# Kernel optimization log

Measured on AMD Instinct MI355X. Metric: run time of the kernel, lower is better.

The kernel has to match this reference:

```python
import jax, jax.numpy as jnp
import numpy as np

B, C, N = 2, 1024, 80
D = 3 * C + 2  # 3074 token dim
DFF = 2048     # torch TransformerEncoderLayer default dim_feedforward
HW = 224
REFINE = 3
EPS = 1e-5


def _layernorm(x, g, b):
    m = jnp.mean(x, axis=-1, keepdims=True)
    v = jnp.mean((x - m) ** 2, axis=-1, keepdims=True)
    return g * (x - m) / jnp.sqrt(v + EPS) + b


def _pos_encoding(seq_len, dim):
    pos = jnp.arange(seq_len, dtype=jnp.float32)[:, None]
    div = jnp.exp(jnp.arange(0, dim, 2, dtype=jnp.float32) * (-np.log(10000.0) / dim))
    pe = jnp.zeros((seq_len, dim), dtype=jnp.float32)
    pe = pe.at[:, 0::2].set(jnp.sin(pos * div)).at[:, 1::2].set(jnp.cos(pos * div))
    return pe


def _forward(pre_f, curr_f, first_f, ln_g, ln_b, ipw, ipb, opw, opb,
             n1g, n1b, l1w, l1b, l2w, l2b, n2g, n2b, ow, ob,
             prev_b, first_b):
    # --- vectorized find_best_shift: batched circular L1 correlation ---
    idx = (jnp.arange(N)[None, :] - jnp.arange(N)[:, None]) % N  # [shift, pos]
    rolled = first_b[:, idx]                                     # [B, N, N, 2]
    dist = jnp.abs(prev_b[:, None] - rolled).sum(axis=(-1, -2))  # [B, N]
    best = jnp.argmin(dist, axis=1)                              # first min, like torch loop
    roll_idx = (jnp.arange(N)[None, :] - best[:, None]) % N      # [B, N]
    first_b = jax.vmap(lambda fb, ri: fb[ri])(first_b, roll_idx)

    # --- bilinear upsample to 224x224 (F.interpolate, align_corners=False) ---
    up = lambda f: jax.image.resize(f, (f.shape[0], f.shape[1], HW, HW), method='bilinear')
    pre_up, curr_up, first_up = up(pre_f), up(curr_f), up(first_f)

    # --- vectorized get_bou_features: [B,N,C] gather ---
    gather = jax.vmap(lambda f, b: f[:, b[:, 0], b[:, 1]].T)
    pre_q = gather(pre_up, prev_b)      # [B, N, C]
    first_q = gather(first_up, first_b)  # [B, N, C]

    pe = _pos_encoding(N, D)
    curr = prev_b.astype(jnp.float32)
    scale = 1.0 / jnp.sqrt(jnp.float32(D))
    results = []
    for _ in range(REFINE):
        bf = gather(curr_up, curr.astype(jnp.int32))          # [B, N, C]
        tokens = jnp.concatenate([pre_q, bf, curr, first_q], axis=-1)  # [B, N, D]
        tokens = _layernorm(tokens, ln_g, ln_b)
        tokens = tokens + pe[None]
        # --- TransformerEncoderLayer (post-norm, nhead=1, relu, eval/no dropout) ---
        qkv = tokens @ ipw.T + ipb
        q, k, v = jnp.split(qkv, 3, axis=-1)
        attn = jax.nn.softmax(jnp.einsum('bqd,bkd->bqk', q, k) * scale, axis=-1)
        a = jnp.einsum('bqk,bkd->bqd', attn, v) @ opw.T + opb
        x = _layernorm(tokens + a, n1g, n1b)
        ff = jax.nn.relu(x @ l1w.T + l1b) @ l2w.T + l2b
        x = _layernorm(x + ff, n2g, n2b)
        out = x @ ow.T + ob                                   # [B, N, 1026]
        curr = jnp.clip(curr + out[..., C:], 0.0, 223.0)
        pre_q = pre_q + out[..., :C]
        results.append(curr)
    return jnp.stack(results)  # [REFINE, B, N, 2]


def setup_inputs() -> dict:
    key = jax.random.key(0)
    ks = jax.random.split(key, 12)
    f = lambda i, s: jax.random.normal(ks[i], s, dtype=jnp.float32)
    w = lambda i, s: 0.02 * jax.random.normal(ks[i], s, dtype=jnp.float32)
    return {
        'pre_img_features': f(0, (B, C, 14, 14)),
        'curr_img_features': f(1, (B, C, 14, 14)),
        'first_img_features': f(2, (B, C, 14, 14)),
        'previous_boundary': jax.random.randint(ks[3], (B, N, 2), 0, HW),
        'first_boundary': jax.random.randint(ks[4], (B, N, 2), 0, HW),
        'ln_g': jnp.ones((D,), jnp.float32), 'ln_b': jnp.zeros((D,), jnp.float32),
        'in_proj_w': w(5, (3 * D, D)), 'in_proj_b': jnp.zeros((3 * D,), jnp.float32),
        'out_proj_w': w(6, (D, D)), 'out_proj_b': jnp.zeros((D,), jnp.float32),
        'norm1_g': jnp.ones((D,), jnp.float32), 'norm1_b': jnp.zeros((D,), jnp.float32),
        'lin1_w': w(7, (DFF, D)), 'lin1_b': jnp.zeros((DFF,), jnp.float32),
        'lin2_w': w(8, (D, DFF)), 'lin2_b': jnp.zeros((D,), jnp.float32),
        'norm2_g': jnp.ones((D,), jnp.float32), 'norm2_b': jnp.zeros((D,), jnp.float32),
        'out_w': w(9, (C + 2, D)), 'out_b': jnp.zeros((C + 2,), jnp.float32),
    }


def reference(pre_img_features, curr_img_features, first_img_features,
              previous_boundary, first_boundary,
              ln_g, ln_b, in_proj_w, in_proj_b, out_proj_w, out_proj_b,
              norm1_g, norm1_b, lin1_w, lin1_b, lin2_w, lin2_b,
              norm2_g, norm2_b, out_w, out_b):
    return _forward(pre_img_features, curr_img_features, first_img_features,
                    ln_g, ln_b, in_proj_w, in_proj_b, out_proj_w, out_proj_b,
                    norm1_g, norm1_b, lin1_w, lin1_b, lin2_w, lin2_b,
                    norm2_g, norm2_b, out_w, out_b,
                    previous_boundary, first_boundary)
```

## Files before the change

kernel.cpp:

```cpp
#include <hip/hip_runtime.h>
#include <math.h>

#define B_    2
#define C_    1024
#define N_    80
#define D_    3074
#define DFF_  2048
#define OD_   1026
#define QKV_  9222
#define M_    160
#define EPS_  1e-5f
#define KPD_  3104

#define SQKV 4
#define PQKV 25
#define SOP  8
#define POP  13
#define SFF1 11
#define PFF1 9
#define SFF2 8
#define PFF2 8
#define SHD  11
#define PHD  9

typedef __attribute__((ext_vector_type(8))) short bf16x8;
typedef __attribute__((ext_vector_type(4))) float f32x4;

__device__ inline short f2bf(float f) {
    unsigned u = __float_as_uint(f);
    u += 0x7fffu + ((u >> 16) & 1u);
    return (short)(u >> 16);
}

__device__ inline int pack2bf(float lo, float hi) {
    return (int)(unsigned short)f2bf(lo) | ((int)(unsigned short)f2bf(hi) << 16);
}

__device__ inline float wave_sum(float v) {
#pragma unroll
    for (int off = 32; off > 0; off >>= 1) v += __shfl_down(v, off, 64);
    return v;
}

__device__ inline void block_reduce_2(float& s, float& s2, float* red) {
    int tid = threadIdx.x;
    int lane = tid & 63, wid = tid >> 6;
    s = wave_sum(s);
    s2 = wave_sum(s2);
    if (lane == 0) { red[wid] = s; red[4 + wid] = s2; }
    __syncthreads();
    if (tid == 0) {
        red[8] = red[0] + red[1] + red[2] + red[3];
        red[9] = red[4] + red[5] + red[6] + red[7];
    }
    __syncthreads();
    s = red[8]; s2 = red[9];
}

__device__ inline void bilin_setup(int p, int& i0, int& i1, float& t) {
    float s = (p + 0.5f) * 0.0625f - 0.5f;
    s = fminf(fmaxf(s, 0.0f), 13.0f);
    i0 = (int)s;
    t = s - (float)i0;
    i1 = min(i0 + 1, 13);
}

__device__ inline float bilin_tap(const float* f, int y0, int y1, float ty,
                                  int x0, int x1, float tx) {
    float a = f[y0 * 14 + x0], b = f[y0 * 14 + x1];
    float c = f[y1 * 14 + x0], d = f[y1 * 14 + x1];
    return (1.f - ty) * ((1.f - tx) * a + tx * b) + ty * ((1.f - tx) * c + tx * d);
}

__global__ __launch_bounds__(128) void align_kernel(const int* __restrict__ prev_b,
                                                    const int* __restrict__ first_b,
                                                    int* __restrict__ fb_al) {
    int b = blockIdx.x;
    int tid = threadIdx.x;
    __shared__ int dist[N_];
    __shared__ int bestIdx;
    if (tid < N_) {
        int s = 0;
        for (int j = 0; j < N_; ++j) {
            int src = (j - tid) % N_;
            if (src < 0) src += N_;
            int dy = prev_b[(b * N_ + j) * 2] - first_b[(b * N_ + src) * 2];
            int dx = prev_b[(b * N_ + j) * 2 + 1] - first_b[(b * N_ + src) * 2 + 1];
            s += abs(dy) + abs(dx);
        }
        dist[tid] = s;
    }
    __syncthreads();
    if (tid == 0) {
        int best = 0, bd = dist[0];
        for (int i = 1; i < N_; ++i)
            if (dist[i] < bd) { bd = dist[i]; best = i; }
        bestIdx = best;
    }
    __syncthreads();
    if (tid < N_) {
        int src = (tid - bestIdx) % N_;
        if (src < 0) src += N_;
        fb_al[(b * N_ + tid) * 2]     = first_b[(b * N_ + src) * 2];
        fb_al[(b * N_ + tid) * 2 + 1] = first_b[(b * N_ + src) * 2 + 1];
    }
}

__global__ __launch_bounds__(256) void gather_init_kernel(
        const float* __restrict__ pre_f, const float* __restrict__ first_f,
        const int* __restrict__ prev_b, const int* __restrict__ fb_al,
        float* __restrict__ pre_q, float* __restrict__ first_q,
        float* __restrict__ curr) {
    int m = blockIdx.x;
    int b = m / N_;
    int tid = threadIdx.x;
    int py = prev_b[m * 2], px = prev_b[m * 2 + 1];
    int fy = fb_al[m * 2], fx = fb_al[m * 2 + 1];
    int py0, py1, px0, px1, fy0, fy1, fx0, fx1;
    float pty, ptx, fty, ftx;
    bilin_setup(py, py0, py1, pty);
    bilin_setup(px, px0, px1, ptx);
    bilin_setup(fy, fy0, fy1, fty);
    bilin_setup(fx, fx0, fx1, ftx);
    for (int c = tid; c < C_; c += 256) {
        const float* fp = pre_f + (size_t)(b * C_ + c) * 196;
        const float* ff = first_f + (size_t)(b * C_ + c) * 196;
        pre_q[(size_t)m * C_ + c]   = bilin_tap(fp, py0, py1, pty, px0, px1, ptx);
        first_q[(size_t)m * C_ + c] = bilin_tap(ff, fy0, fy1, fty, fx0, fx1, ftx);
    }
    if (tid < 2) curr[m * 2 + tid] = (float)prev_b[m * 2 + tid];
}

__global__ __launch_bounds__(256) void pe_kernel(float* __restrict__ pe) {
    int n = blockIdx.x;
    const float negLogDivD = -logf(10000.0f) / (float)D_;
    for (int d = threadIdx.x; d < D_; d += 256) {
        int kk = d >> 1;
        float ang = (float)n * expf((float)(2 * kk) * negLogDivD);
        pe[(size_t)n * D_ + d] = (d & 1) ? cosf(ang) : sinf(ang);
    }
}

__global__ __launch_bounds__(256) void tokens_kernel(
        const float* __restrict__ curr_f, const float* __restrict__ pre_q,
        const float* __restrict__ first_q, const float* __restrict__ curr,
        const float* __restrict__ ln_g, const float* __restrict__ ln_b,
        const float* __restrict__ pe_tab,
        float* __restrict__ tokens, short* __restrict__ tokens_bf) {
    int m = blockIdx.x;
    int b = m / N_;
    int n = m % N_;
    int tid = threadIdx.x;
    __shared__ float bf[C_];
    __shared__ float red[10];

    float cy = curr[m * 2], cx = curr[m * 2 + 1];
    int iy = (int)cy, ix = (int)cx;
    int y0, y1, x0, x1;
    float ty, tx;
    bilin_setup(iy, y0, y1, ty);
    bilin_setup(ix, x0, x1, tx);
    for (int c = tid; c < C_; c += 256) {
        const float* f = curr_f + (size_t)(b * C_ + c) * 196;
        bf[c] = bilin_tap(f, y0, y1, ty, x0, x1, tx);
    }
    __syncthreads();

    float s = 0.f, s2 = 0.f;
    for (int d = tid; d < D_; d += 256) {
        float v;
        if (d < C_)            v = pre_q[(size_t)m * C_ + d];
        else if (d < 2 * C_)   v = bf[d - C_];
        else if (d == 2 * C_)  v = cy;
        else if (d == 2*C_+1)  v = cx;
        else                   v = first_q[(size_t)m * C_ + (d - 2 * C_ - 2)];
        s += v; s2 += v * v;
    }
    block_reduce_2(s, s2, red);
    float mean = s / (float)D_;
    float var = s2 / (float)D_ - mean * mean;
    float inv = rsqrtf(var + EPS_);

    for (int d = tid; d < KPD_; d += 256) {
        if (d < D_) {
            float v;
            if (d < C_)            v = pre_q[(size_t)m * C_ + d];
            else if (d < 2 * C_)   v = bf[d - C_];
            else if (d == 2 * C_)  v = cy;
            else if (d == 2*C_+1)  v = cx;
            else                   v = first_q[(size_t)m * C_ + (d - 2 * C_ - 2)];
            float ln = ln_g[d] * (v - mean) * inv + ln_b[d];
            float val = ln + pe_tab[(size_t)n * D_ + d];
            tokens[(size_t)m * D_ + d] = val;
            tokens_bf[(size_t)m * KPD_ + d] = f2bf(val);
        } else {
            tokens_bf[(size_t)m * KPD_ + d] = 0;
        }
    }
}

__global__ __launch_bounds__(256) void wpack2(const float* __restrict__ w,
                                              short* __restrict__ o,
                                              int K, int O, int nch, int ntiles) {
    int gw = (int)((blockIdx.x * 256 + threadIdx.x) >> 6);
    if (gw >= ntiles) return;
    int lane = threadIdx.x & 63;
    int strip = gw / nch, chunk = gw - strip * nch;
    int row = strip * 16 + (lane >> 2);
    int k0 = chunk * 32 + (lane & 3) * 8;
    float f[8];
    if (row < O && k0 + 8 <= K) {
        const float* src = w + (size_t)row * K + k0;
        float2 a = *(const float2*)(src);
        float2 b = *(const float2*)(src + 2);
        float2 c = *(const float2*)(src + 4);
        float2 d = *(const float2*)(src + 6);
        f[0]=a.x; f[1]=a.y; f[2]=b.x; f[3]=b.y;
        f[4]=c.x; f[5]=c.y; f[6]=d.x; f[7]=d.y;
    } else {
#pragma unroll
        for (int j = 0; j < 8; ++j) {
            int k = k0 + j;
            f[j] = (row < O && k < K) ? w[(size_t)row * K + k] : 0.f;
        }
    }
    int p0 = pack2bf(f[0], f[1]);
    int p1 = pack2bf(f[2], f[3]);
    int p2 = pack2bf(f[4], f[5]);
    int p3 = pack2bf(f[6], f[7]);
    int src = (lane & 15) * 4 + (lane >> 4);
    int4 out;
    out.x = __shfl(p0, src, 64);
    out.y = __shfl(p1, src, 64);
    out.z = __shfl(p2, src, 64);
    out.w = __shfl(p3, src, 64);
    *(int4*)(o + (size_t)gw * 512 + (size_t)lane * 8) = out;
}

template <int SW>
__global__ __launch_bounds__(512) void gemm_stage(
        const short* __restrict__ A, const short* __restrict__ Wp,
        const float* __restrict__ bias, float* __restrict__ part,
        int KpA, int nch, int O, int per) {
    int cs = blockIdx.y * per;
    int ce = min(nch, cs + per);
    if (cs >= ce) return;
    int tid = threadIdx.x;
    int lane = tid & 63, wave = tid >> 6;
    int col = lane & 15, quad = lane >> 4;
    int s0 = (blockIdx.x * 8 + wave) * SW;

    __shared__ short lbuf[2][160 * 32];

    int m0 = tid >> 2, p8 = (tid & 3) * 8;
    int m1 = (tid + 512) >> 2;
    const short* a0 = A + (size_t)m0 * KpA + p8;
    const short* a1 = A + (size_t)m1 * KpA + p8;
    bf16x8 sr0, sr1;

    f32x4 acc[SW][10];
#pragma unroll
    for (int j = 0; j < SW; ++j)
#pragma unroll
        for (int t = 0; t < 10; ++t)
#pragma unroll
            for (int r = 0; r < 4; ++r) acc[j][t][r] = 0.f;

    const short* wbase[SW];
#pragma unroll
    for (int j = 0; j < SW; ++j)
        wbase[j] = Wp + (size_t)(s0 + j) * nch * 512 + (size_t)lane * 8;
    bf16x8 wc[SW], wn[SW];

    sr0 = *(const bf16x8*)(a0 + (size_t)cs * 32);
    if (tid < 128) sr1 = *(const bf16x8*)(a1 + (size_t)cs * 32);
#pragma unroll
    for (int j = 0; j < SW; ++j)
        wc[j] = *(const bf16x8*)(wbase[j] + (size_t)cs * 512);
    *(bf16x8*)(&lbuf[0][m0 * 32 + p8]) = sr0;
    if (tid < 128) *(bf16x8*)(&lbuf[0][m1 * 32 + p8]) = sr1;
    __syncthreads();

    int cur = 0;
    for (int c = cs; c < ce; ++c) {
        bool more = (c + 1) < ce;
        if (more) {
            sr0 = *(const bf16x8*)(a0 + (size_t)(c + 1) * 32);
            if (tid < 128) sr1 = *(const bf16x8*)(a1 + (size_t)(c + 1) * 32);
#pragma unroll
            for (int j = 0; j < SW; ++j)
                wn[j] = *(const bf16x8*)(wbase[j] + (size_t)(c + 1) * 512);
        }
#pragma unroll
        for (int t = 0; t < 10; ++t) {
            bf16x8 af = *(const bf16x8*)(&lbuf[cur][t * 512 + col * 32 + quad * 8]);
#pragma unroll
            for (int j = 0; j < SW; ++j)
                acc[j][t] = __builtin_amdgcn_mfma_f32_16x16x32_bf16(af, wc[j], acc[j][t], 0, 0, 0);
        }
        if (more) {
            *(bf16x8*)(&lbuf[cur ^ 1][m0 * 32 + p8]) = sr0;
            if (tid < 128) *(bf16x8*)(&lbuf[cur ^ 1][m1 * 32 + p8]) = sr1;
        }
        __syncthreads();
#pragma unroll
        for (int j = 0; j < SW; ++j) wc[j] = wn[j];
        cur ^= 1;
    }

    float* pout = part + (size_t)blockIdx.y * M_ * O;
#pragma unroll
    for (int j = 0; j < SW; ++j) {
        int oc = (s0 + j) * 16 + col;
        if (oc < O) {
            float bv = (blockIdx.y == 0) ? bias[oc] : 0.f;
#pragma unroll
            for (int t = 0; t < 10; ++t)
#pragma unroll
                for (int r = 0; r < 4; ++r)
                    pout[(size_t)(t * 16 + quad * 4 + r) * O + oc] = acc[j][t][r] + bv;
        }
    }
}

__global__ __launch_bounds__(256) void gemm_mfma_sk(
        const short* __restrict__ A, const float* __restrict__ Wf,
        const float* __restrict__ bias, float* __restrict__ Cout,
        int K, int KpA, int O, int KC) {
    int kc0 = blockIdx.y * KC;
    if (kc0 >= K) return;
    int kend = min(K, kc0 + KC);

    int lane = threadIdx.x & 63;
    int wave = threadIdx.x >> 6;
    int col  = lane & 15;
    int quad = lane >> 4;
    int o0 = blockIdx.x * 128 + wave * 32 + col;
    int o1 = o0 + 16;
    int oc0 = min(o0, O - 1), oc1 = min(o1, O - 1);

    const float* wrow0 = Wf + (size_t)oc0 * K + quad * 8;
    const float* wrow1 = Wf + (size_t)oc1 * K + quad * 8;
    const short* abase = A + (size_t)col * KpA + quad * 8;

    f32x4 acc0[10], acc1[10];
#pragma unroll
    for (int t = 0; t < 10; ++t)
#pragma unroll
        for (int r = 0; r < 4; ++r) { acc0[t][r] = 0.f; acc1[t][r] = 0.f; }

    int nfull = (kend - kc0) >> 5;
    bf16x8 aCur[10];
    float2 wCur[8];
    if (nfull > 0) {
#pragma unroll
        for (int t = 0; t < 10; ++t)
            aCur[t] = *(const bf16x8*)(abase + (size_t)t * 16 * KpA + kc0);
#pragma unroll
        for (int j = 0; j < 4; ++j) {
            wCur[j]     = *(const float2*)(wrow0 + kc0 + 2 * j);
            wCur[4 + j] = *(const float2*)(wrow1 + kc0 + 2 * j);
        }
    }
    for (int i = 0; i < nfull; ++i) {
        bf16x8 aNxt[10];
        float2 wNxt[8];
        if (i + 1 < nfull) {
            int kn = kc0 + (i + 1) * 32;
#pragma unroll
            for (int t = 0; t < 10; ++t)
                aNxt[t] = *(const bf16x8*)(abase + (size_t)t * 16 * KpA + kn);
#pragma unroll
            for (int j = 0; j < 4; ++j) {
                wNxt[j]     = *(const float2*)(wrow0 + kn + 2 * j);
                wNxt[4 + j] = *(const float2*)(wrow1 + kn + 2 * j);
            }
        }
        bf16x8 b0, b1;
#pragma unroll
        for (int j = 0; j < 4; ++j) {
            b0[2*j] = f2bf(wCur[j].x);     b0[2*j+1] = f2bf(wCur[j].y);
            b1[2*j] = f2bf(wCur[4+j].x);   b1[2*j+1] = f2bf(wCur[4+j].y);
        }
#pragma unroll
        for (int t = 0; t < 10; ++t) {
            acc0[t] = __builtin_amdgcn_mfma_f32_16x16x32_bf16(aCur[t], b0, acc0[t], 0, 0, 0);
            acc1[t] = __builtin_amdgcn_mfma_f32_16x16x32_bf16(aCur[t], b1, acc1[t], 0, 0, 0);
        }
#pragma unroll
        for (int t = 0; t < 10; ++t) aCur[t] = aNxt[t];
#pragma unroll
        for (int j = 0; j < 8; ++j) wCur[j] = wNxt[j];
    }
    int kmain = kc0 + nfull * 32;
    if (kmain < kend) {
        bf16x8 b0, b1;
#pragma unroll
        for (int j = 0; j < 8; ++j) {
            int k = kmain + quad * 8 + j;
            b0[j] = (k < kend) ? f2bf(Wf[(size_t)oc0 * K + k]) : (short)0;
            b1[j] = (k < kend) ? f2bf(Wf[(size_t)oc1 * K + k]) : (short)0;
        }
#pragma unroll
        for (int t = 0; t < 10; ++t) {
            bf16x8 af = *(const bf16x8*)(abase + (size_t)t * 16 * KpA + kmain);
            acc0[t] = __builtin_amdgcn_mfma_f32_16x16x32_bf16(af, b0, acc0[t], 0, 0, 0);
            acc1[t] = __builtin_amdgcn_mfma_f32_16x16x32_bf16(af, b1, acc1[t], 0, 0, 0);
        }
    }
    if (o0 < O) {
        float bv = (blockIdx.y == 0) ? bias[o0] : 0.f;
#pragma unroll
        for (int t = 0; t < 10; ++t)
#pragma unroll
            for (int r = 0; r < 4; ++r)
                atomicAdd(&Cout[(size_t)(t * 16 + quad * 4 + r) * O + o0], acc0[t][r] + bv);
    }
    if (o1 < O) {
        float bv = (blockIdx.y == 0) ? bias[o1] : 0.f;
#pragma unroll
        for (int t = 0; t < 10; ++t)
#pragma unroll
            for (int r = 0; r < 4; ++r)
                atomicAdd(&Cout[(size_t)(t * 16 + quad * 4 + r) * O + o1], acc1[t][r] + bv);
    }
}

__global__ __launch_bounds__(256) void relu_cvt_kernel(const float* __restrict__ in,
                                                       int S, size_t sstr,
                                                       short* __restrict__ out,
                                                       int n) {
    int i = blockIdx.x * 256 + threadIdx.x;
    if (i < n) {
        float v = 0.f;
        for (int s = 0; s < S; ++s) v += in[(size_t)s * sstr + i];
        out[i] = f2bf(fmaxf(v, 0.f));
    }
}

__global__ __launch_bounds__(256) void qkv_cvt_kernel(const float* __restrict__ part,
                                                      int S,
                                                      short* __restrict__ q_bf,
                                                      short* __restrict__ k_bf,
                                                      short* __restrict__ v_bf) {
    int mb = blockIdx.x;
    int b = mb / 96, q = mb % 96;
    if (q >= N_) {
        for (int d = threadIdx.x; d < KPD_; d += 256)
            v_bf[((size_t)b * 96 + q) * KPD_ + d] = 0;
        return;
    }
    int m = b * N_ + q;
    for (int d = threadIdx.x; d < KPD_; d += 256) {
        short qv = 0, kv = 0, vv = 0;
        if (d < D_) {
            float qf = 0.f, kf = 0.f, vf = 0.f;
            for (int s = 0; s < S; ++s) {
                const float* p = part + (size_t)s * M_ * QKV_ + (size_t)m * QKV_;
                qf += p[d]; kf += p[D_ + d]; vf += p[2 * D_ + d];
            }
            qv = f2bf(qf); kv = f2bf(kf); vv = f2bf(vf);
        }
        q_bf[(size_t)m * KPD_ + d] = qv;
        k_bf[(size_t)m * KPD_ + d] = kv;
        v_bf[((size_t)b * 96 + q) * KPD_ + d] = vv;
    }
}

__global__ __launch_bounds__(256) void attn_sc(const short* __restrict__ q_bf,
                                               const short* __restrict__ k_bf,
                                               short* __restrict__ p_bf) {
    int bi = blockIdx.x;
    int b = bi / 5, qt = bi % 5;
    int lane = threadIdx.x & 63, wave = threadIdx.x >> 6;
    int col = lane & 15, quad = lane >> 4;
    const short* qbase = q_bf + (size_t)(b * N_ + qt * 16 + col) * KPD_ + quad * 8;
    const short* kb = k_bf + (size_t)(b * N_ + col) * KPD_ + quad * 8;

    f32x4 acc[5];
#pragma unroll
    for (int kt = 0; kt < 5; ++kt)
#pragma unroll
        for (int r = 0; r < 4; ++r) acc[kt][r] = 0.f;

    int c0 = wave * 25, c1 = min(97, c0 + 25);
    for (int c = c0; c < c1; ++c) {
        bf16x8 af = *(const bf16x8*)(qbase + (size_t)c * 32);
#pragma unroll
        for (int kt = 0; kt < 5; ++kt) {
            bf16x8 kf = *(const bf16x8*)(kb + (size_t)(kt * 16) * KPD_ + (size_t)c * 32);
            acc[kt] = __builtin_amdgcn_mfma_f32_16x16x32_bf16(af, kf, acc[kt], 0, 0, 0);
        }
    }

    __shared__ f32x4 red[4][5][64];
    __shared__ float sl[16][80];
#pragma unroll
    for (int kt = 0; kt < 5; ++kt) red[wave][kt][lane] = acc[kt];
    __syncthreads();
    float scale = rsqrtf((float)D_);
    for (int item = threadIdx.x; item < 320; item += 256) {
        int kt = item >> 6, l2 = item & 63;
        int c2 = l2 & 15, q2 = l2 >> 4;
        f32x4 v = red[0][kt][l2];
#pragma unroll
        for (int w = 1; w < 4; ++w)
#pragma unroll
            for (int r = 0; r < 4; ++r) v[r] += red[w][kt][l2][r];
#pragma unroll
        for (int r = 0; r < 4; ++r)
            sl[q2 * 4 + r][kt * 16 + c2] = v[r] * scale;
    }
    __syncthreads();

    int r = wave * 4 + (lane >> 4);
    int cb = lane & 15;
    float v[5];
    float mx = -1e30f;
#pragma unroll
    for (int i = 0; i < 5; ++i) { v[i] = sl[r][cb + 16 * i]; mx = fmaxf(mx, v[i]); }
#pragma unroll
    for (int off = 1; off < 16; off <<= 1) mx = fmaxf(mx, __shfl_xor(mx, off, 64));
    float e[5];
    float sum = 0.f;
#pragma unroll
    for (int i = 0; i < 5; ++i) { e[i] = expf(v[i] - mx); sum += e[i]; }
#pragma unroll
    for (int off = 1; off < 16; off <<= 1) sum += __shfl_xor(sum, off, 64);
    float rs = 1.0f / sum;
    size_t m96 = (size_t)(b * N_ + qt * 16 + r) * 96;
#pragma unroll
    for (int i = 0; i < 5; ++i) p_bf[m96 + cb + 16 * i] = f2bf(e[i] * rs);
    p_bf[m96 + 80 + cb] = 0;
}

__global__ __launch_bounds__(256) void av_mfma(const short* __restrict__ p_bf,
                                               const short* __restrict__ v_bf,
                                               short* __restrict__ av_bf) {
    int bi = blockIdx.x;
    int b = bi / 49, g = bi % 49;
    int lane = threadIdx.x & 63, wave = threadIdx.x >> 6;
    int dtile = g * 4 + wave;
    if (dtile >= 194) return;
    int d0 = dtile * 16;
    int col = lane & 15, quad = lane >> 4;
    const short* pbase = p_bf + (size_t)b * N_ * 96 + quad * 8;
    const short* vb = v_bf + (size_t)b * 96 * KPD_ + d0 + col;
    f32x4 acc[5];
#pragma unroll
    for (int t = 0; t < 5; ++t)
#pragma unroll
        for (int r = 0; r < 4; ++r) acc[t][r] = 0.f;
#pragma unroll
    for (int c = 0; c < 3; ++c) {
        bf16x8 bf8;
#pragma unroll
        for (int j = 0; j < 8; ++j)
            bf8[j] = vb[(size_t)(c * 32 + quad * 8 + j) * KPD_];
#pragma unroll
        for (int t = 0; t < 5; ++t) {
            bf16x8 af = *(const bf16x8*)(pbase + (size_t)(t * 16 + col) * 96 + c * 32);
            acc[t] = __builtin_amdgcn_mfma_f32_16x16x32_bf16(af, bf8, acc[t], 0, 0, 0);
        }
    }
#pragma unroll
    for (int t = 0; t < 5; ++t)
#pragma unroll
        for (int r = 0; r < 4; ++r)
            av_bf[(size_t)(b * N_ + t * 16 + quad * 4 + r) * KPD_ + d0 + col] = f2bf(acc[t][r]);
}

template <bool WF32>
__global__ __launch_bounds__(256) void ln_kernel(const float* __restrict__ xin,
                                                 int S, size_t sstr,
                                                 const float* __restrict__ res,
                                                 const float* __restrict__ g,
                                                 const float* __restrict__ bta,
                                                 float* __restrict__ outf,
                                                 short* __restrict__ outb) {
    int m = blockIdx.x;
    int tid = threadIdx.x;
    __shared__ float red[10];
    const float* xr = xin + (size_t)m * D_;
    const float* rr = res + (size_t)m * D_;
    float vv[13];
    float s = 0.f, s2 = 0.f;
#pragma unroll
    for (int i = 0; i < 13; ++i) {
        int d = tid + i * 256;
        float v = 0.f;
        if (d < D_) {
            v = rr[d];
            for (int sp = 0; sp < S; ++sp) v += xr[(size_t)sp * sstr + d];
            s += v; s2 += v * v;
        }
        vv[i] = v;
    }
    block_reduce_2(s, s2, red);
    float mean = s / (float)D_;
    float var = s2 / (float)D_ - mean * mean;
    float inv = rsqrtf(var + EPS_);
#pragma unroll
    for (int i = 0; i < 13; ++i) {
        int d = tid + i * 256;
        if (d < D_) {
            float y = g[d] * (vv[i] - mean) * inv + bta[d];
            if (WF32) outf[(size_t)m * D_ + d] = y;
            outb[(size_t)m * KPD_ + d] = f2bf(y);
        } else if (d < KPD_) {
            outb[(size_t)m * KPD_ + d] = 0;
        }
    }
}

__global__ __launch_bounds__(256) void update_kernel(const float* __restrict__ part,
                                                     int S, size_t sstr,
                                                     float* __restrict__ curr,
                                                     float* __restrict__ pre_q,
                                                     float* __restrict__ results) {
    int m = blockIdx.x;
    int tid = threadIdx.x;
    const float* pr = part + (size_t)m * OD_;
    for (int c = tid; c < C_; c += 256) {
        float v = 0.f;
        for (int s = 0; s < S; ++s) v += pr[(size_t)s * sstr + c];
        pre_q[(size_t)m * C_ + c] += v;
    }
    if (tid < 2) {
        float v = 0.f;
        for (int s = 0; s < S; ++s) v += pr[(size_t)s * sstr + C_ + tid];
        float nc = curr[m * 2 + tid] + v;
        nc = fminf(fmaxf(nc, 0.f), 223.f);
        curr[m * 2 + tid] = nc;
        results[m * 2 + tid] = nc;
    }
}

extern "C" void kernel_launch(void* const* d_in, const int* in_sizes, int n_in,
                              void* d_out, int out_size, void* d_ws, size_t ws_size,
                              hipStream_t stream) {
    const float* pre_f   = (const float*)d_in[0];
    const float* curr_f  = (const float*)d_in[1];
    const float* first_f = (const float*)d_in[2];
    const int*   prev_b  = (const int*)d_in[3];
    const int*   first_b = (const int*)d_in[4];
    const float* ln_g    = (const float*)d_in[5];
    const float* ln_b    = (const float*)d_in[6];
    const float* ipw     = (const float*)d_in[7];
    const float* ipb     = (const float*)d_in[8];
    const float* opw     = (const float*)d_in[9];
    const float* opb     = (const float*)d_in[10];
    const float* n1g     = (const float*)d_in[11];
    const float* n1b     = (const float*)d_in[12];
    const float* l1w     = (const float*)d_in[13];
    const float* l1b     = (const float*)d_in[14];
    const float* l2w     = (const float*)d_in[15];
    const float* l2b     = (const float*)d_in[16];
    const float* n2g     = (const float*)d_in[17];
    const float* n2b     = (const float*)d_in[18];
    const float* ow      = (const float*)d_in[19];
    const float* ob      = (const float*)d_in[20];
    float* outp = (float*)d_out;

    float* wf = (float*)d_ws;
    size_t off = 0;
    int*   fb_al   = (int*)(wf + off); off += 320;
    float* curr    = wf + off;         off += 320;
    float* pre_q   = wf + off;         off += (size_t)M_ * C_;
    float* first_q = wf + off;         off += (size_t)M_ * C_;
    float* tokens  = wf + off;         off += (size_t)M_ * D_;
    float* xbuf    = wf + off;         off += (size_t)M_ * D_;
    float* pe_tab  = wf + off;         off += (size_t)N_ * D_;
    short* tokens_bf = (short*)(wf + off); off += (size_t)M_ * KPD_ / 2;
    short* x_bf      = (short*)(wf + off); off += (size_t)M_ * KPD_ / 2;
    short* x2_bf     = (short*)(wf + off); off += (size_t)M_ * KPD_ / 2;
    short* av_bf     = (short*)(wf + off); off += (size_t)M_ * KPD_ / 2;
    short* ff1_bf    = (short*)(wf + off); off += (size_t)M_ * DFF_ / 2;
    short* q_bf      = (short*)(wf + off); off += (size_t)M_ * KPD_ / 2;
    short* k_bf      = (short*)(wf + off); off += (size_t)M_ * KPD_ / 2;
    short* v_bf      = (short*)(wf + off); off += (size_t)B_ * 96 * KPD_ / 2;
    short* p_bf      = (short*)(wf + off); off += (size_t)M_ * 96 / 2;
    size_t commonF = off;

    size_t o2 = commonF;
    short* ipw_p2 = (short*)(wf + o2); o2 += (size_t)592 * 97 * 256;
    short* opw_p2 = (short*)(wf + o2); o2 += (size_t)208 * 97 * 256;
    short* l1w_p2 = (short*)(wf + o2); o2 += (size_t)128 * 97 * 256;
    short* l2w_p2 = (short*)(wf + o2); o2 += (size_t)208 * 64 * 256;
    short* ow_p2  = (short*)(wf + o2); o2 += (size_t)80  * 97 * 256;
    float* gpart  = wf + o2;           o2 += (size_t)SQKV * M_ * QKV_;

    size_t o0 = commonF;
    float* qkv   = wf + o0; o0 += (size_t)M_ * QKV_;
    float* aout  = wf + o0; o0 += (size_t)M_ * D_;
    float* ff1f  = wf + o0; o0 += (size_t)M_ * DFF_;
    float* ffout = wf + o0; o0 += (size_t)M_ * D_;
    float* outb  = wf + o0; o0 += (size_t)M_ * OD_;

    int tier = (ws_size >= o2 * sizeof(float)) ? 2 : 0;
    (void)in_sizes; (void)n_in; (void)out_size;

    hipLaunchKernelGGL(align_kernel, dim3(B_), dim3(128), 0, stream,
                       prev_b, first_b, fb_al);
    hipLaunchKernelGGL(gather_init_kernel, dim3(M_), dim3(256), 0, stream,
                       pre_f, first_f, prev_b, fb_al, pre_q, first_q, curr);
    hipLaunchKernelGGL(pe_kernel, dim3(N_), dim3(256), 0, stream, pe_tab);

    if (tier == 2) {
        hipLaunchKernelGGL(wpack2, dim3(592 * 97 / 4), dim3(256), 0, stream,
                           ipw, ipw_p2, D_, QKV_, 97, 592 * 97);
        hipLaunchKernelGGL(wpack2, dim3(208 * 97 / 4), dim3(256), 0, stream,
                           opw, opw_p2, D_, D_, 97, 208 * 97);
        hipLaunchKernelGGL(wpack2, dim3(128 * 97 / 4), dim3(256), 0, stream,
                           l1w, l1w_p2, D_, DFF_, 97, 128 * 97);
        hipLaunchKernelGGL(wpack2, dim3(208 * 64 / 4), dim3(256), 0, stream,
                           l2w, l2w_p2, DFF_, D_, 64, 208 * 64);
        hipLaunchKernelGGL(wpack2, dim3(80 * 97 / 4), dim3(256), 0, stream,
                           ow, ow_p2, D_, OD_, 97, 80 * 97);
    }

    for (int it = 0; it < 3; ++it) {
        if (tier == 0) {
            hipMemsetAsync(qkv,   0, (size_t)M_ * QKV_ * 4, stream);
            hipMemsetAsync(aout,  0, (size_t)M_ * D_   * 4, stream);
            hipMemsetAsync(ff1f,  0, (size_t)M_ * DFF_ * 4, stream);
            hipMemsetAsync(ffout, 0, (size_t)M_ * D_   * 4, stream);
            hipMemsetAsync(outb,  0, (size_t)M_ * OD_  * 4, stream);
        }

        hipLaunchKernelGGL(tokens_kernel, dim3(M_), dim3(256), 0, stream,
                           curr_f, pre_q, first_q, curr, ln_g, ln_b, pe_tab,
                           tokens, tokens_bf);
        if (tier == 2)
            hipLaunchKernelGGL((gemm_stage<2>), dim3(37, SQKV), dim3(512), 0, stream,
                               tokens_bf, ipw_p2, ipb, gpart, KPD_, 97, QKV_, PQKV);
        else
            hipLaunchKernelGGL(gemm_mfma_sk, dim3(73, 6), dim3(256), 0, stream,
                               tokens_bf, ipw, ipb, qkv, D_, KPD_, QKV_, 544);
        hipLaunchKernelGGL(qkv_cvt_kernel, dim3(B_ * 96), dim3(256), 0, stream,
                           (tier == 2) ? gpart : qkv, (tier == 2) ? SQKV : 1,
                           q_bf, k_bf, v_bf);
        hipLaunchKernelGGL(attn_sc, dim3(B_ * 5), dim3(256), 0, stream,
                           q_bf, k_bf, p_bf);
        hipLaunchKernelGGL(av_mfma, dim3(98), dim3(256), 0, stream,
                           p_bf, v_bf, av_bf);
        if (tier == 2)
            hipLaunchKernelGGL((gemm_stage<2>), dim3(13, SOP), dim3(512), 0, stream,
                               av_bf, opw_p2, opb, gpart, KPD_, 97, D_, POP);
        else
            hipLaunchKernelGGL(gemm_mfma_sk, dim3(25, 10), dim3(256), 0, stream,
                               av_bf, opw, opb, aout, D_, KPD_, D_, 320);
        hipLaunchKernelGGL((ln_kernel<true>), dim3(M_), dim3(256), 0, stream,
                           (tier == 2) ? gpart : aout, (tier == 2) ? SOP : 1, (size_t)M_ * D_,
                           tokens, n1g, n1b, xbuf, x_bf);
        if (tier == 2)
            hipLaunchKernelGGL((gemm_stage<2>), dim3(8, SFF1), dim3(512), 0, stream,
                               x_bf, l1w_p2, l1b, gpart, KPD_, 97, DFF_, PFF1);
        else
            hipLaunchKernelGGL(gemm_mfma_sk, dim3(16, 17), dim3(256), 0, stream,
                               x_bf, l1w, l1b, ff1f, D_, KPD_, DFF_, 192);
        hipLaunchKernelGGL(relu_cvt_kernel, dim3((M_ * DFF_ + 255) / 256), dim3(256), 0, stream,
                           (tier == 2) ? gpart : ff1f, (tier == 2) ? SFF1 : 1, (size_t)M_ * DFF_,
                           ff1_bf, M_ * DFF_);
        if (tier == 2)
            hipLaunchKernelGGL((gemm_stage<2>), dim3(13, SFF2), dim3(512), 0, stream,
                               ff1_bf, l2w_p2, l2b, gpart, DFF_, 64, D_, PFF2);
        else
            hipLaunchKernelGGL(gemm_mfma_sk, dim3(25, 11), dim3(256), 0, stream,
                               ff1_bf, l2w, l2b, ffout, DFF_, DFF_, D_, 192);
        hipLaunchKernelGGL((ln_kernel<false>), dim3(M_), dim3(256), 0, stream,
                           (tier == 2) ? gpart : ffout, (tier == 2) ? SFF2 : 1, (size_t)M_ * D_,
                           xbuf, n2g, n2b, (float*)nullptr, x2_bf);
        if (tier == 2)
            hipLaunchKernelGGL((gemm_stage<2>), dim3(5, SHD), dim3(512), 0, stream,
                               x2_bf, ow_p2, ob, gpart, KPD_, 97, OD_, PHD);
        else
            hipLaunchKernelGGL(gemm_mfma_sk, dim3(9, 13), dim3(256), 0, stream,
                               x2_bf, ow, ob, outb, D_, KPD_, OD_, 256);
        hipLaunchKernelGGL(update_kernel, dim3(M_), dim3(256), 0, stream,
                           (tier == 2) ? gpart : outb, (tier == 2) ? SHD : 1, (size_t)M_ * OD_,
                           curr, pre_q, outp + (size_t)it * M_ * 2);
    }
}
```

Before: 1.022 ms.

## Fuse softmax with AV, pad GEMM LDS rows, cache token values in registers

Three changes. First, the attention score/softmax kernel and the AV matmul are merged into one kernel that keeps probabilities in shared memory, removing a launch and the p_bf round trip. The fused kernel runs only 10 blocks, so far fewer waves do the AV work than the previous 98-block launch. Second, the GEMM stage's LDS A-tile row stride is padded from 32 to 36 shorts to reduce bank conflicts on MFMA operand reads. Third, the tokens kernel keeps the gathered values in registers between the statistics and normalize passes instead of reloading them.

Measured after the change: 1.117 ms. 9.3% more time.

```diff
diff --git a/kernel.cpp b/kernel.cpp
--- a/kernel.cpp
+++ b/kernel.cpp
@@ -11,6 +11,7 @@
 #define M_    160
 #define EPS_  1e-5f
 #define KPD_  3104
+#define ASTR  36
 
 #define SQKV 4
 #define PQKV 25
@@ -166,34 +167,36 @@
     }
     __syncthreads();
 
+    float vv[13];
     float s = 0.f, s2 = 0.f;
-    for (int d = tid; d < D_; d += 256) {
-        float v;
-        if (d < C_)            v = pre_q[(size_t)m * C_ + d];
-        else if (d < 2 * C_)   v = bf[d - C_];
-        else if (d == 2 * C_)  v = cy;
-        else if (d == 2*C_+1)  v = cx;
-        else                   v = first_q[(size_t)m * C_ + (d - 2 * C_ - 2)];
-        s += v; s2 += v * v;
-    }
-    block_reduce_2(s, s2, red);
-    float mean = s / (float)D_;
-    float var = s2 / (float)D_ - mean * mean;
-    float inv = rsqrtf(var + EPS_);
-
-    for (int d = tid; d < KPD_; d += 256) {
+#pragma unroll
+    for (int i = 0; i < 13; ++i) {
+        int d = tid + i * 256;
+        float v = 0.f;
         if (d < D_) {
-            float v;
             if (d < C_)            v = pre_q[(size_t)m * C_ + d];
             else if (d < 2 * C_)   v = bf[d - C_];
             else if (d == 2 * C_)  v = cy;
             else if (d == 2*C_+1)  v = cx;
             else                   v = first_q[(size_t)m * C_ + (d - 2 * C_ - 2)];
-            float ln = ln_g[d] * (v - mean) * inv + ln_b[d];
+            s += v; s2 += v * v;
+        }
+        vv[i] = v;
+    }
+    block_reduce_2(s, s2, red);
+    float mean = s / (float)D_;
+    float var = s2 / (float)D_ - mean * mean;
+    float inv = rsqrtf(var + EPS_);
+
+#pragma unroll
+    for (int i = 0; i < 13; ++i) {
+        int d = tid + i * 256;
+        if (d < D_) {
+            float ln = ln_g[d] * (vv[i] - mean) * inv + ln_b[d];
             float val = ln + pe_tab[(size_t)n * D_ + d];
             tokens[(size_t)m * D_ + d] = val;
             tokens_bf[(size_t)m * KPD_ + d] = f2bf(val);
-        } else {
+        } else if (d < KPD_) {
             tokens_bf[(size_t)m * KPD_ + d] = 0;
         }
     }
@@ -250,7 +253,7 @@
     int col = lane & 15, quad = lane >> 4;
     int s0 = (blockIdx.x * 8 + wave) * SW;
 
-    __shared__ short lbuf[2][160 * 32];
+    __shared__ short lbuf[2][160 * ASTR];
 
     int m0 = tid >> 2, p8 = (tid & 3) * 8;
     int m1 = (tid + 512) >> 2;
@@ -277,8 +280,8 @@
 #pragma unroll
     for (int j = 0; j < SW; ++j)
         wc[j] = *(const bf16x8*)(wbase[j] + (size_t)cs * 512);
-    *(bf16x8*)(&lbuf[0][m0 * 32 + p8]) = sr0;
-    if (tid < 128) *(bf16x8*)(&lbuf[0][m1 * 32 + p8]) = sr1;
+    *(bf16x8*)(&lbuf[0][m0 * ASTR + p8]) = sr0;
+    if (tid < 128) *(bf16x8*)(&lbuf[0][m1 * ASTR + p8]) = sr1;
     __syncthreads();
 
     int cur = 0;
@@ -293,14 +296,14 @@
         }
 #pragma unroll
         for (int t = 0; t < 10; ++t) {
-            bf16x8 af = *(const bf16x8*)(&lbuf[cur][t * 512 + col * 32 + quad * 8]);
+            bf16x8 af = *(const bf16x8*)(&lbuf[cur][(t * 16 + col) * ASTR + quad * 8]);
 #pragma unroll
             for (int j = 0; j < SW; ++j)
                 acc[j][t] = __builtin_amdgcn_mfma_f32_16x16x32_bf16(af, wc[j], acc[j][t], 0, 0, 0);
         }
         if (more) {
-            *(bf16x8*)(&lbuf[cur ^ 1][m0 * 32 + p8]) = sr0;
-            if (tid < 128) *(bf16x8*)(&lbuf[cur ^ 1][m1 * 32 + p8]) = sr1;
+            *(bf16x8*)(&lbuf[cur ^ 1][m0 * ASTR + p8]) = sr0;
+            if (tid < 128) *(bf16x8*)(&lbuf[cur ^ 1][m1 * ASTR + p8]) = sr1;
         }
         __syncthreads();
 #pragma unroll
@@ -467,9 +470,10 @@
     }
 }
 
-__global__ __launch_bounds__(256) void attn_sc(const short* __restrict__ q_bf,
+__global__ __launch_bounds__(256) void attn_av(const short* __restrict__ q_bf,
                                                const short* __restrict__ k_bf,
-                                               short* __restrict__ p_bf) {
+                                               const short* __restrict__ v_bf,
+                                               short* __restrict__ av_bf) {
     int bi = blockIdx.x;
     int b = bi / 5, qt = bi % 5;
     int lane = threadIdx.x & 63, wave = threadIdx.x >> 6;
@@ -495,6 +499,7 @@
 
     __shared__ f32x4 red[4][5][64];
     __shared__ float sl[16][80];
+    __shared__ short p_s[16][104];
 #pragma unroll
     for (int kt = 0; kt < 5; ++kt) red[wave][kt][lane] = acc[kt];
     __syncthreads();
@@ -513,61 +518,49 @@
     }
     __syncthreads();
 
-    int r = wave * 4 + (lane >> 4);
-    int cb = lane & 15;
-    float v[5];
-    float mx = -1e30f;
-#pragma unroll
-    for (int i = 0; i < 5; ++i) { v[i] = sl[r][cb + 16 * i]; mx = fmaxf(mx, v[i]); }
-#pragma unroll
-    for (int off = 1; off < 16; off <<= 1) mx = fmaxf(mx, __shfl_xor(mx, off, 64));
-    float e[5];
-    float sum = 0.f;
-#pragma unroll
-    for (int i = 0; i < 5; ++i) { e[i] = expf(v[i] - mx); sum += e[i]; }
-#pragma unroll
-    for (int off = 1; off < 16; off <<= 1) sum += __shfl_xor(sum, off, 64);
-    float rs = 1.0f / sum;
-    size_t m96 = (size_t)(b * N_ + qt * 16 + r) * 96;
-#pragma unroll
-    for (int i = 0; i < 5; ++i) p_bf[m96 + cb + 16 * i] = f2bf(e[i] * rs);
-    p_bf[m96 + 80 + cb] = 0;
-}
-
-__global__ __launch_bounds__(256) void av_mfma(const short* __restrict__ p_bf,
-                                               const short* __restrict__ v_bf,
-                                               short* __restrict__ av_bf) {
-    int bi = blockIdx.x;
-    int b = bi / 49, g = bi % 49;
-    int lane = threadIdx.x & 63, wave = threadIdx.x >> 6;
-    int dtile = g * 4 + wave;
-    if (dtile >= 194) return;
-    int d0 = dtile * 16;
-    int col = lane & 15, quad = lane >> 4;
-    const short* pbase = p_bf + (size_t)b * N_ * 96 + quad * 8;
-    const short* vb = v_bf + (size_t)b * 96 * KPD_ + d0 + col;
-    f32x4 acc[5];
-#pragma unroll
-    for (int t = 0; t < 5; ++t)
-#pragma unroll
-        for (int r = 0; r < 4; ++r) acc[t][r] = 0.f;
-#pragma unroll
-    for (int c = 0; c < 3; ++c) {
-        bf16x8 bf8;
-#pragma unroll
-        for (int j = 0; j < 8; ++j)
-            bf8[j] = vb[(size_t)(c * 32 + quad * 8 + j) * KPD_];
-#pragma unroll
-        for (int t = 0; t < 5; ++t) {
-            bf16x8 af = *(const bf16x8*)(pbase + (size_t)(t * 16 + col) * 96 + c * 32);
-            acc[t] = __builtin_amdgcn_mfma_f32_16x16x32_bf16(af, bf8, acc[t], 0, 0, 0);
-        }
-    }
-#pragma unroll
-    for (int t = 0; t < 5; ++t)
+    {
+        int r = wave * 4 + (lane >> 4);
+        int cb = lane & 15;
+        float v[5];
+        float mx = -1e30f;
+#pragma unroll
+        for (int i = 0; i < 5; ++i) { v[i] = sl[r][cb + 16 * i]; mx = fmaxf(mx, v[i]); }
+#pragma unroll
+        for (int off = 1; off < 16; off <<= 1) mx = fmaxf(mx, __shfl_xor(mx, off, 64));
+        float e[5];
+        float sum = 0.f;
+#pragma unroll
+        for (int i = 0; i < 5; ++i) { e[i] = expf(v[i] - mx); sum += e[i]; }
+#pragma unroll
+        for (int off = 1; off < 16; off <<= 1) sum += __shfl_xor(sum, off, 64);
+        float rs = 1.0f / sum;
+#pragma unroll
+        for (int i = 0; i < 5; ++i) p_s[r][cb + 16 * i] = f2bf(e[i] * rs);
+        p_s[r][80 + cb] = 0;
+        if (cb < 8) p_s[r][96 + cb] = 0;
+    }
+    __syncthreads();
+
+    const short* vb0 = v_bf + (size_t)b * 96 * KPD_ + col;
+    for (int dt = wave; dt < 194; dt += 4) {
+        int d0 = dt * 16;
+        const short* vb = vb0 + d0;
+        f32x4 a2;
+#pragma unroll
+        for (int r = 0; r < 4; ++r) a2[r] = 0.f;
+#pragma unroll
+        for (int c = 0; c < 3; ++c) {
+            bf16x8 vf;
+#pragma unroll
+            for (int j = 0; j < 8; ++j)
+                vf[j] = vb[(size_t)(c * 32 + quad * 8 + j) * KPD_];
+            bf16x8 pf = *(const bf16x8*)(&p_s[col][c * 32 + quad * 8]);
+            a2 = __builtin_amdgcn_mfma_f32_16x16x32_bf16(pf, vf, a2, 0, 0, 0);
+        }
 #pragma unroll
         for (int r = 0; r < 4; ++r)
-            av_bf[(size_t)(b * N_ + t * 16 + quad * 4 + r) * KPD_ + d0 + col] = f2bf(acc[t][r]);
+            av_bf[(size_t)(b * N_ + qt * 16 + quad * 4 + r) * KPD_ + d0 + col] = f2bf(a2[r]);
+    }
 }
 
 template <bool WF32>
@@ -679,7 +672,6 @@
     short* q_bf      = (short*)(wf + off); off += (size_t)M_ * KPD_ / 2;
     short* k_bf      = (short*)(wf + off); off += (size_t)M_ * KPD_ / 2;
     short* v_bf      = (short*)(wf + off); off += (size_t)B_ * 96 * KPD_ / 2;
-    short* p_bf      = (short*)(wf + off); off += (size_t)M_ * 96 / 2;
     size_t commonF = off;
 
     size_t o2 = commonF;
@@ -731,19 +723,19 @@
         hipLaunchKernelGGL(tokens_kernel, dim3(M_), dim3(256), 0, stream,
                            curr_f, pre_q, first_q, curr, ln_g, ln_b, pe_tab,
                            tokens, tokens_bf);
-        if (tier == 2)
+        if (tier == 2) {
             hipLaunchKernelGGL((gemm_stage<2>), dim3(37, SQKV), dim3(512), 0, stream,
                                tokens_bf, ipw_p2, ipb, gpart, KPD_, 97, QKV_, PQKV);
-        else
+            hipLaunchKernelGGL(qkv_cvt_kernel, dim3(B_ * 96), dim3(256), 0, stream,
+                               gpart, SQKV, q_bf, k_bf, v_bf);
+        } else {
             hipLaunchKernelGGL(gemm_mfma_sk, dim3(73, 6), dim3(256), 0, stream,
                                tokens_bf, ipw, ipb, qkv, D_, KPD_, QKV_, 544);
-        hipLaunchKernelGGL(qkv_cvt_kernel, dim3(B_ * 96), dim3(256), 0, stream,
-                           (tier == 2) ? gpart : qkv, (tier == 2) ? SQKV : 1,
-                           q_bf, k_bf, v_bf);
-        hipLaunchKernelGGL(attn_sc, dim3(B_ * 5), dim3(256), 0, stream,
-                           q_bf, k_bf, p_bf);
-        hipLaunchKernelGGL(av_mfma, dim3(98), dim3(256), 0, stream,
-                           p_bf, v_bf, av_bf);
+            hipLaunchKernelGGL(qkv_cvt_kernel, dim3(B_ * 96), dim3(256), 0, stream,
+                               qkv, 1, q_bf, k_bf, v_bf);
+        }
+        hipLaunchKernelGGL(attn_av, dim3(B_ * 5), dim3(256), 0, stream,
+                           q_bf, k_bf, v_bf, av_bf);
         if (tier == 2)
             hipLaunchKernelGGL((gemm_stage<2>), dim3(13, SOP), dim3(512), 0, stream,
                                av_bf, opw_p2, opb, gpart, KPD_, 97, D_, POP);
```
